# Kernel optimization log

Hardware: AMD Instinct MI355X
Metric: run time of the kernel (lower is better)

The kernel has to match this reference:

```python
import jax, jax.numpy as jnp
import numpy as np

V, D, H, FF, L, ER_LEN = 267, 512, 8, 1024, 6, 2048
HD = D // H
NEG = -1e9


def sinusoidal_pe(S, d, dtype):
    pos = np.arange(S)[:, None].astype(np.float32)
    div = np.exp(np.arange(0, d, 2).astype(np.float32) * (-np.log(10000.0) / d))
    pe = np.zeros((S, d), dtype=np.float32)
    pe[:, 0::2] = np.sin(pos * div)
    pe[:, 1::2] = np.cos(pos * div)
    return jnp.asarray(pe, dtype=dtype)[:, None, :]  # [S,1,D]


def layernorm(x, g, b, eps=1e-5):
    mu = jnp.mean(x, -1, keepdims=True)
    var = jnp.var(x, -1, keepdims=True)
    return (x - mu) * jax.lax.rsqrt(var + eps) * g + b


def skew(qe):
    # qe: [B,H,S,S] -> Music-Transformer skew producing srel [B,H,S,S]
    S = qe.shape[-1]
    mask = jnp.flip(jnp.triu(jnp.ones((S, S), qe.dtype)), axis=0)
    qe = qe * mask
    qe = jnp.pad(qe, ((0, 0), (0, 0), (0, 0), (1, 0)))
    qe = qe.reshape(qe.shape[0], qe.shape[1], S + 1, S)
    return qe[:, :, 1:, :]


def setup_inputs() -> dict:
    key = jax.random.key(0)
    ks = jax.random.split(key, 20)
    s = 0.02
    inp = {
        'inputs_seq': jax.random.randint(ks[0], (2, 2048), 0, V),
        'emb': jax.random.normal(ks[1], (V, D)) * s,
        'in_proj_w': jax.random.normal(ks[2], (L, 3 * D, D)) * s,
        'in_proj_b': jnp.zeros((L, 3 * D)),
        'out_proj_w': jax.random.normal(ks[3], (L, D, D)) * s,
        'out_proj_b': jnp.zeros((L, D)),
        'er': jax.random.normal(ks[4], (L, ER_LEN, HD)) * s,
        'lin1_w': jax.random.normal(ks[5], (L, FF, D)) * s,
        'lin1_b': jnp.zeros((L, FF)),
        'lin2_w': jax.random.normal(ks[6], (L, D, FF)) * s,
        'lin2_b': jnp.zeros((L, D)),
        'ln1_g': jnp.ones((L, D)), 'ln1_b': jnp.zeros((L, D)),
        'ln2_g': jnp.ones((L, D)), 'ln2_b': jnp.zeros((L, D)),
        'fln_g': jnp.ones((D,)), 'fln_b': jnp.zeros((D,)),
        'wout_w': jax.random.normal(ks[7], (V, D)) * s,
        'wout_b': jnp.zeros((V,)),
    }
    return inp


def reference(inputs_seq, emb, in_proj_w, in_proj_b, out_proj_w, out_proj_b, er,
              lin1_w, lin1_b, lin2_w, lin2_b, ln1_g, ln1_b, ln2_g, ln2_b,
              fln_g, fln_b, wout_w, wout_b):
    B, S = inputs_seq.shape
    x = emb[inputs_seq]                       # [B,S,D]
    x = jnp.transpose(x, (1, 0, 2))           # [S,B,D] seq-first
    x = x + sinusoidal_pe(S, D, x.dtype)
    causal = jnp.triu(jnp.full((S, S), NEG, x.dtype), k=1)
    er_start = max(0, ER_LEN - S)
    scale = 1.0 / jnp.sqrt(jnp.asarray(HD, x.dtype))

    for i in range(L):
        qkv = jnp.einsum('sbd,ed->sbe', x, in_proj_w[i]) + in_proj_b[i]
        q, k, v = jnp.split(qkv, 3, axis=-1)
        # [S,B,D] -> [B,H,S,hd]
        def heads(t):
            return jnp.transpose(t.reshape(S, B, H, HD), (1, 2, 0, 3))
        q, k, v = heads(q) * scale, heads(k), heads(v)
        scores = jnp.einsum('bhqd,bhkd->bhqk', q, k)
        qe = jnp.einsum('bhqd,ed->bhqe', q, er[i][er_start:])
        scores = scores + skew(qe) + causal
        attn = jax.nn.softmax(scores, axis=-1)
        ctx = jnp.einsum('bhqk,bhkd->bhqd', attn, v)
        ctx = jnp.transpose(ctx, (2, 0, 1, 3)).reshape(S, B, D)
        attn_out = jnp.einsum('sbd,ed->sbe', ctx, out_proj_w[i]) + out_proj_b[i]
        x = layernorm(x + attn_out, ln1_g[i], ln1_b[i])
        h = jax.nn.relu(jnp.einsum('sbd,fd->sbf', x, lin1_w[i]) + lin1_b[i])
        ff = jnp.einsum('sbf,df->sbd', h, lin2_w[i]) + lin2_b[i]
        x = layernorm(x + ff, ln2_g[i], ln2_b[i])

    x = layernorm(x, fln_g, fln_b)
    return jnp.einsum('sbd,vd->sbv', x, wout_w) + wout_b  # [S,B,V]
```

## Files before the change

### kernel.cpp

```cpp
#include <hip/hip_runtime.h>
#include <hip/hip_bf16.h>

typedef __attribute__((ext_vector_type(4))) float f32x4;
typedef __attribute__((ext_vector_type(8))) short bf16x8;
typedef __attribute__((ext_vector_type(2))) unsigned short u16x2;
typedef __attribute__((ext_vector_type(4))) unsigned short u16x4;
typedef __attribute__((ext_vector_type(8))) unsigned short u16x8;

#define S_LEN 2048
#define BATCH 2
#define DMODEL 512
#define NHEAD 8
#define HDIM 64
#define MROWS 4096
#define LAYERS 6

#define MFMA16(a, b, c) __builtin_amdgcn_mfma_f32_16x16x32_bf16((a), (b), (c), 0, 0, 0)

__device__ __forceinline__ float bf2f(unsigned short u) {
    return __uint_as_float(((unsigned)u) << 16);
}
__device__ __forceinline__ unsigned short f2bf(float f) {
    union { float f; unsigned u; } v; v.f = f;
    unsigned r = v.u + 0x7FFF + ((v.u >> 16) & 1);
    return (unsigned short)(r >> 16);
}
__device__ __forceinline__ bf16x8 load8(const unsigned short* p) {
    return *reinterpret_cast<const bf16x8*>(p);
}

__global__ __launch_bounds__(256) void f2bf_kernel(
    const float* __restrict__ src, unsigned short* __restrict__ dst, int n8)
{
    int i = blockIdx.x * 256 + threadIdx.x;
    if (i >= n8) return;
    f32x4 a = *reinterpret_cast<const f32x4*>(src + (size_t)i * 8);
    f32x4 b = *reinterpret_cast<const f32x4*>(src + (size_t)i * 8 + 4);
    u16x8 o;
#pragma unroll
    for (int j = 0; j < 4; ++j) { o[j] = f2bf(a[j]); o[4 + j] = f2bf(b[j]); }
    *reinterpret_cast<u16x8*>(dst + (size_t)i * 8) = o;
}

__global__ __launch_bounds__(256) void embed_pe_kernel(
    const int* __restrict__ seq, const float* __restrict__ emb,
    float* __restrict__ x, unsigned short* __restrict__ x16)
{
    const int r = blockIdx.x;
    const int j = threadIdx.x;
    const int s = r >> 1, b = r & 1;
    const int tok = seq[b * S_LEN + s];
    const float e0 = emb[(size_t)tok * DMODEL + 2 * j];
    const float e1 = emb[(size_t)tok * DMODEL + 2 * j + 1];
    const double c = -9.210340371976184 / 512.0;
    double dv = exp((double)(2 * j) * c);
    double arg = (double)s * dv;
    const float v0 = e0 + (float)sin(arg);
    const float v1 = e1 + (float)cos(arg);
    x[(size_t)r * DMODEL + 2 * j]     = v0;
    x[(size_t)r * DMODEL + 2 * j + 1] = v1;
    u16x2 o; o[0] = f2bf(v0); o[1] = f2bf(v1);
    *reinterpret_cast<u16x2*>(x16 + (size_t)r * DMODEL + 2 * j) = o;
}

template<int BM>
__global__ __launch_bounds__(256) void gemm_mfma_kernel(
    const unsigned short* __restrict__ A, const unsigned short* __restrict__ W,
    const float* __restrict__ bias,
    float* __restrict__ Cf, unsigned short* __restrict__ Cb,
    unsigned short* __restrict__ vT,
    int N, int K, int relu, int qkvsplit)
{
    constexpr int MF = BM / 32;
    __shared__ __align__(16) unsigned short As[BM * 64];
    __shared__ __align__(16) unsigned short Bs[64 * 64];
    const int tid = threadIdx.x;
    const int w = tid >> 6, lane = tid & 63, l15 = lane & 15, hi = lane >> 4;
    const int wm = w >> 1, wn = w & 1;
    const int n0 = blockIdx.x * 64, m0 = blockIdx.y * BM;
    const int sr = tid >> 3;
    const int ss = tid & 7;

    bf16x8 aprf[MF], bprf[2];
    auto loadA = [&](int k0) {
#pragma unroll
        for (int i = 0; i < MF; ++i) {
            const int r = sr + 32 * i;
            aprf[i] = load8(A + (size_t)(m0 + r) * K + k0 + ((ss ^ ((r >> 1) & 7)) * 8));
        }
    };
    auto loadB = [&](int k0) {
#pragma unroll
        for (int i = 0; i < 2; ++i) {
            const int r = sr + 32 * i;
            const int nn = n0 + r;
            if (nn < N) bprf[i] = load8(W + (size_t)nn * K + k0 + ((ss ^ ((r >> 1) & 7)) * 8));
            else { u16x8 z = {0,0,0,0,0,0,0,0}; bprf[i] = *reinterpret_cast<bf16x8*>(&z); }
        }
    };

    f32x4 acc[MF][2];
#pragma unroll
    for (int mf = 0; mf < MF; ++mf)
#pragma unroll
        for (int nf = 0; nf < 2; ++nf) acc[mf][nf] = f32x4{0.f, 0.f, 0.f, 0.f};

    loadA(0); loadB(0);
    for (int k0 = 0; k0 < K; k0 += 64) {
        __syncthreads();
#pragma unroll
        for (int i = 0; i < MF; ++i)
            *reinterpret_cast<bf16x8*>(As + (sr + 32 * i) * 64 + ss * 8) = aprf[i];
#pragma unroll
        for (int i = 0; i < 2; ++i)
            *reinterpret_cast<bf16x8*>(Bs + (sr + 32 * i) * 64 + ss * 8) = bprf[i];
        if (k0 + 64 < K) { loadA(k0 + 64); loadB(k0 + 64); }
        __syncthreads();

        bf16x8 af[MF][2], bfr[2][2];
#pragma unroll
        for (int mf = 0; mf < MF; ++mf) {
            const int r = wm * (BM / 2) + mf * 16 + l15;
            const int sw = (r >> 1) & 7;
            const unsigned short* base = As + r * 64;
            af[mf][0] = *reinterpret_cast<const bf16x8*>(base + ((hi ^ sw) * 8));
            af[mf][1] = *reinterpret_cast<const bf16x8*>(base + (((hi + 4) ^ sw) * 8));
        }
#pragma unroll
        for (int nf = 0; nf < 2; ++nf) {
            const int r = wn * 32 + nf * 16 + l15;
            const int sw = (r >> 1) & 7;
            const unsigned short* base = Bs + r * 64;
            bfr[nf][0] = *reinterpret_cast<const bf16x8*>(base + ((hi ^ sw) * 8));
            bfr[nf][1] = *reinterpret_cast<const bf16x8*>(base + (((hi + 4) ^ sw) * 8));
        }
#pragma unroll
        for (int mf = 0; mf < MF; ++mf)
#pragma unroll
            for (int nf = 0; nf < 2; ++nf) {
                acc[mf][nf] = MFMA16(af[mf][0], bfr[nf][0], acc[mf][nf]);
                acc[mf][nf] = MFMA16(af[mf][1], bfr[nf][1], acc[mf][nf]);
            }
    }

#pragma unroll
    for (int nf = 0; nf < 2; ++nf) {
        const int col = n0 + wn * 32 + nf * 16 + l15;
        const bool okc = col < N;
        const float bv = okc ? bias[col] : 0.f;
#pragma unroll
        for (int mf = 0; mf < MF; ++mf) {
            const int rbase = m0 + wm * (BM / 2) + mf * 16 + hi * 4;
#pragma unroll
            for (int rg = 0; rg < 4; ++rg) {
                float v = acc[mf][nf][rg] + bv;
                if (relu) v = fmaxf(v, 0.f);
                if (okc) {
                    const int row = rbase + rg;
                    if (qkvsplit) {
                        if (col < 1024) {
                            if (col < 512) v *= 0.125f;
                            Cb[(size_t)row * 1024 + col] = f2bf(v);
                        } else {
                            const int h = (col - 1024) >> 6, d = (col - 1024) & 63;
                            const int s = row >> 1, bb = row & 1;
                            const int kt = s >> 6, kin = s & 63;
                            const int pos = (kin & 3) | (((kin >> 4) & 1) << 2)
                                          | (((kin >> 2) & 3) << 3) | (kin & 32);
                            vT[((((size_t)(bb * 8 + h) * 32 + kt) * 64 + d) << 6) + pos] = f2bf(v);
                        }
                    } else {
                        const size_t idx = (size_t)row * N + col;
                        if (Cb) Cb[idx] = f2bf(v);
                        else    Cf[idx] = v;
                    }
                }
            }
        }
    }
}

__global__ __launch_bounds__(256, 2) void attn_mfma_kernel(
    const unsigned short* __restrict__ qk16, const unsigned short* __restrict__ vT16,
    const unsigned short* __restrict__ er16,
    unsigned short* __restrict__ part16, float* __restrict__ mlbuf)
{
    __shared__ __align__(16) unsigned short K_s[64 * 64];
    __shared__ __align__(16) unsigned short V_T[64 * 64];
    __shared__ __align__(16) unsigned short Er_s[64 * 64];
    __shared__ __align__(16) unsigned short E_w[4 * 16 * 196];

    const int tid  = threadIdx.x;
    const int w    = tid >> 6;
    const int lane = tid & 63;
    const int l15  = lane & 15;
    const int hi   = lane >> 4;
    const int bx   = blockIdx.y;
    const int bh   = blockIdx.x;
    const int b    = bh >> 3, hh = bh & 7;
    const int sk   = lane;
    const int dg0  = w;
    const int dv0  = 16 * w + (lane >> 3);
    const int gv   = lane & 7;

    int qb, c;
    if (bx < 32) { qb = 31 - (bx >> 1); c = bx & 1; }
    else         { qb = 15 - (bx - 32); c = 0; }
    const int pidx = bh * 48 + bx;
    const int q0   = qb * 64;
    const int k0s  = c * 1024;
    const int ntl  = min(qb + 1 - c * 16, 16);
    const int qg   = q0 + 16 * w + l15;

    const unsigned short* qptr = qk16 + ((size_t)qg * BATCH + b) * 1024 + hh * HDIM;
    bf16x8 qf0 = load8(qptr + hi * 8);
    bf16x8 qf1 = load8(qptr + 32 + hi * 8);

    unsigned short* ewp = E_w + (w * 16 + l15) * 196;
    const int E0  = 1984 - q0 + k0s;
    const int E0m = E0 % 192;

#pragma unroll 2
    for (int mf = 0; mf < 8; ++mf) {
        int e = E0 + mf * 16 + l15;
        int ec = e > 2047 ? 2047 : e;
        bf16x8 a0 = load8(er16 + (size_t)ec * 64 + hi * 8);
        bf16x8 a1 = load8(er16 + (size_t)ec * 64 + 32 + hi * 8);
        f32x4 acc = {0.f, 0.f, 0.f, 0.f};
        acc = MFMA16(a0, qf0, acc);
        acc = MFMA16(a1, qf1, acc);
        int col = E0m + mf * 16 + 4 * hi;
        if (col >= 192) col -= 192;
        u16x4 ew;
#pragma unroll
        for (int r = 0; r < 4; ++r) ew[r] = f2bf(acc[r]);
        *reinterpret_cast<u16x4*>(ewp + col) = ew;
    }

    float m = -INFINITY, lsum = 0.f;
    f32x4 acc_o[4];
#pragma unroll
    for (int mf = 0; mf < 4; ++mf) acc_o[mf] = f32x4{0.f, 0.f, 0.f, 0.f};

    int col0t = (2047 - qg + k0s) % 192;

    bf16x8 kpr0, kpr1, vpr0, vpr1, epr0, epr1;
    {
        const unsigned short* krow = qk16 + ((size_t)(k0s + sk) * BATCH + b) * 1024 + 512 + hh * HDIM;
        kpr0 = load8(krow + dg0 * 8);       kpr1 = load8(krow + (dg0 + 4) * 8);
        const unsigned short* vbase = vT16 + (((size_t)bh * 32 + (k0s >> 6)) * 64) * 64;
        vpr0 = load8(vbase + dv0 * 64 + gv * 8);
        vpr1 = load8(vbase + (dv0 + 8) * 64 + gv * 8);
    }
    if (ntl > 1) {
        int e = E0 + 128 + sk;
        int ec = e > 2047 ? 2047 : e;
        epr0 = load8(er16 + (size_t)ec * 64 + dg0 * 8);
        epr1 = load8(er16 + (size_t)ec * 64 + (dg0 + 4) * 8);
    }

    for (int t = 0; t < ntl; ++t) {
        const int k0 = k0s + t * 64;
        const bool doE = (t + 1 < ntl);
        __syncthreads();
        *reinterpret_cast<bf16x8*>(K_s + sk * 64 + ((dg0 ^ (sk & 7)) * 8)) = kpr0;
        *reinterpret_cast<bf16x8*>(K_s + sk * 64 + (((dg0 + 4) ^ (sk & 7)) * 8)) = kpr1;
        *reinterpret_cast<bf16x8*>(V_T + dv0 * 64 + ((gv ^ (dv0 & 7)) * 8)) = vpr0;
        *reinterpret_cast<bf16x8*>(V_T + (dv0 + 8) * 64 + ((gv ^ (dv0 & 7)) * 8)) = vpr1;
        if (doE) {
            *reinterpret_cast<bf16x8*>(Er_s + sk * 64 + ((dg0 ^ (sk & 7)) * 8)) = epr0;
            *reinterpret_cast<bf16x8*>(Er_s + sk * 64 + (((dg0 + 4) ^ (sk & 7)) * 8)) = epr1;
        }
        if (t + 1 < ntl) {
            const unsigned short* krow = qk16 + ((size_t)(k0 + 64 + sk) * BATCH + b) * 1024 + 512 + hh * HDIM;
            kpr0 = load8(krow + dg0 * 8);       kpr1 = load8(krow + (dg0 + 4) * 8);
            const unsigned short* vbase = vT16 + (((size_t)bh * 32 + ((k0 + 64) >> 6)) * 64) * 64;
            vpr0 = load8(vbase + dv0 * 64 + gv * 8);
            vpr1 = load8(vbase + (dv0 + 8) * 64 + gv * 8);
            if (t + 2 < ntl) {
                int e = E0 + 128 + 64 * (t + 1) + sk;
                int ec = e > 2047 ? 2047 : e;
                epr0 = load8(er16 + (size_t)ec * 64 + dg0 * 8);
                epr1 = load8(er16 + (size_t)ec * 64 + (dg0 + 4) * 8);
            }
        }
        __syncthreads();

        f32x4 sacc[4];
#pragma unroll
        for (int f = 0; f < 4; ++f) {
            const int row = l15 + 16 * f;
            bf16x8 ka0 = *reinterpret_cast<const bf16x8*>(K_s + row * 64 + (((0 + hi) ^ (l15 & 7)) * 8));
            bf16x8 ka1 = *reinterpret_cast<const bf16x8*>(K_s + row * 64 + (((4 + hi) ^ (l15 & 7)) * 8));
            f32x4 z = {0.f, 0.f, 0.f, 0.f};
            z = MFMA16(ka0, qf0, z);
            sacc[f] = MFMA16(ka1, qf1, z);
        }

        if (doE) {
            const int fbm = (E0 + 128 + 64 * t) % 192;
#pragma unroll
            for (int mf = 0; mf < 4; ++mf) {
                const int rr = l15 + 16 * mf;
                bf16x8 a0 = *reinterpret_cast<const bf16x8*>(Er_s + rr * 64 + ((hi ^ (l15 & 7)) * 8));
                bf16x8 a1 = *reinterpret_cast<const bf16x8*>(Er_s + rr * 64 + (((hi + 4) ^ (l15 & 7)) * 8));
                f32x4 acc = {0.f, 0.f, 0.f, 0.f};
                acc = MFMA16(a0, qf0, acc);
                acc = MFMA16(a1, qf1, acc);
                int col = fbm + mf * 16 + 4 * hi;
                u16x4 ew;
#pragma unroll
                for (int r = 0; r < 4; ++r) ew[r] = f2bf(acc[r]);
                *reinterpret_cast<u16x4*>(ewp + col) = ew;
            }
        }

        float mt = -INFINITY;
#pragma unroll
        for (int f = 0; f < 4; ++f) {
#pragma unroll
            for (int r = 0; r < 4; ++r) {
                const int kk = 16 * f + 4 * hi + r;
                int col = col0t + kk;
                if (col >= 192) col -= 192;
                float sv = sacc[f][r] + bf2f(ewp[col]);
                if (k0 + kk > qg) sv = -1e9f;
                sacc[f][r] = sv;
                mt = fmaxf(mt, sv);
            }
        }
        mt = fmaxf(mt, __shfl_xor(mt, 16));
        mt = fmaxf(mt, __shfl_xor(mt, 32));
        const float mn = fmaxf(m, mt);
        const float corr = __expf(m - mn);
        float ps = 0.f;
#pragma unroll
        for (int f = 0; f < 4; ++f)
#pragma unroll
            for (int r = 0; r < 4; ++r) {
                const float e = __expf(sacc[f][r] - mn);
                sacc[f][r] = e; ps += e;
            }
        ps += __shfl_xor(ps, 16);
        ps += __shfl_xor(ps, 32);
        lsum = lsum * corr + ps;
        m = mn;

        bf16x8 pf0, pf1;
#pragma unroll
        for (int j = 0; j < 8; ++j) {
            pf0[j] = (short)f2bf(sacc[j >> 2][j & 3]);
            pf1[j] = (short)f2bf(sacc[(j >> 2) + 2][j & 3]);
        }

#pragma unroll
        for (int mf = 0; mf < 4; ++mf) {
            f32x4 a = acc_o[mf];
            a[0] *= corr; a[1] *= corr; a[2] *= corr; a[3] *= corr;
            const unsigned short* vrow = V_T + (l15 + 16 * mf) * 64;
            const int sw = l15 & 7;
            bf16x8 vf0 = *reinterpret_cast<const bf16x8*>(vrow + ((hi ^ sw) * 8));
            bf16x8 vf1 = *reinterpret_cast<const bf16x8*>(vrow + (((4 + hi) ^ sw) * 8));
            a = MFMA16(vf0, pf0, a);
            a = MFMA16(vf1, pf1, a);
            acc_o[mf] = a;
        }

        col0t += 64;
        if (col0t >= 192) col0t -= 192;
    }

    unsigned short* pa = part16 + ((size_t)pidx * 64 + 16 * w + l15) * 64;
#pragma unroll
    for (int mf = 0; mf < 4; ++mf) {
        u16x4 o;
#pragma unroll
        for (int r = 0; r < 4; ++r) o[r] = f2bf(acc_o[mf][r]);
        *reinterpret_cast<u16x4*>(pa + 16 * mf + 4 * hi) = o;
    }
    if (hi == 0) {
        float* ml = mlbuf + ((size_t)pidx * 64 + 16 * w + l15) * 2;
        ml[0] = m; ml[1] = lsum;
    }
}

__global__ __launch_bounds__(256) void attn_combine_kernel(
    const unsigned short* __restrict__ part16, const float* __restrict__ mlbuf,
    unsigned short* __restrict__ ctx16)
{
    const int flat = blockIdx.x * 256 + threadIdx.x;
    const int qi = flat >> 3, dg = flat & 7;
    const int bh = qi >> 11, ql = qi & 2047;
    const int b = bh >> 3, hh = bh & 7;
    const int qb = ql >> 6, rl = ql & 63;

    float o[8];
    u16x8 res;
    if (qb >= 16) {
        const int i0 = bh * 48 + 2 * (31 - qb);
        const int i1 = i0 + 1;
        u16x8 a0 = *reinterpret_cast<const u16x8*>(part16 + ((size_t)i0 * 64 + rl) * 64 + dg * 8);
        u16x8 a1 = *reinterpret_cast<const u16x8*>(part16 + ((size_t)i1 * 64 + rl) * 64 + dg * 8);
        const float* ml0 = mlbuf + ((size_t)i0 * 64 + rl) * 2;
        const float* ml1 = mlbuf + ((size_t)i1 * 64 + rl) * 2;
        const float m0 = ml0[0], l0 = ml0[1], m1 = ml1[0], l1 = ml1[1];
        const float ms = fmaxf(m0, m1);
        const float w0 = __expf(m0 - ms), w1 = __expf(m1 - ms);
        const float inv = 1.f / (l0 * w0 + l1 * w1);
#pragma unroll
        for (int j = 0; j < 8; ++j)
            o[j] = (bf2f(a0[j]) * w0 + bf2f(a1[j]) * w1) * inv;
    } else {
        const int i0 = bh * 48 + 32 + (15 - qb);
        u16x8 a0 = *reinterpret_cast<const u16x8*>(part16 + ((size_t)i0 * 64 + rl) * 64 + dg * 8);
        const float inv = 1.f / mlbuf[((size_t)i0 * 64 + rl) * 2 + 1];
#pragma unroll
        for (int j = 0; j < 8; ++j) o[j] = bf2f(a0[j]) * inv;
    }
#pragma unroll
    for (int j = 0; j < 8; ++j) res[j] = f2bf(o[j]);
    *reinterpret_cast<u16x8*>(ctx16 + ((size_t)ql * BATCH + b) * DMODEL + hh * HDIM + dg * 8) = res;
}

__global__ __launch_bounds__(256) void ln_kernel(
    const float* __restrict__ xin, const float* __restrict__ res,
    const float* __restrict__ gg, const float* __restrict__ bb,
    float* __restrict__ xout, unsigned short* __restrict__ x16out, int has_res)
{
    const int w = threadIdx.x >> 6, lane = threadIdx.x & 63;
    const int row = blockIdx.x * 4 + w;
    const float* xp = xin + (size_t)row * DMODEL + lane * 8;
    f32x4 v0 = *reinterpret_cast<const f32x4*>(xp);
    f32x4 v1 = *reinterpret_cast<const f32x4*>(xp + 4);
    if (has_res) {
        const float* rp = res + (size_t)row * DMODEL + lane * 8;
        v0 += *reinterpret_cast<const f32x4*>(rp);
        v1 += *reinterpret_cast<const f32x4*>(rp + 4);
    }
    float sum = 0.f, ssq = 0.f;
#pragma unroll
    for (int c2 = 0; c2 < 4; ++c2) {
        sum += v0[c2] + v1[c2];
        ssq += v0[c2] * v0[c2] + v1[c2] * v1[c2];
    }
#pragma unroll
    for (int off = 32; off > 0; off >>= 1) {
        sum += __shfl_xor(sum, off);
        ssq += __shfl_xor(ssq, off);
    }
    const float mu = sum * (1.f / 512.f);
    const float var = ssq * (1.f / 512.f) - mu * mu;
    const float rstd = rsqrtf(var + 1e-5f);
    f32x4 g0 = *reinterpret_cast<const f32x4*>(gg + lane * 8);
    f32x4 g1 = *reinterpret_cast<const f32x4*>(gg + lane * 8 + 4);
    f32x4 b0 = *reinterpret_cast<const f32x4*>(bb + lane * 8);
    f32x4 b1 = *reinterpret_cast<const f32x4*>(bb + lane * 8 + 4);
    f32x4 o0, o1;
    u16x8 h;
#pragma unroll
    for (int c2 = 0; c2 < 4; ++c2) {
        o0[c2] = (v0[c2] - mu) * rstd * g0[c2] + b0[c2];
        o1[c2] = (v1[c2] - mu) * rstd * g1[c2] + b1[c2];
        h[c2] = f2bf(o0[c2]); h[4 + c2] = f2bf(o1[c2]);
    }
    float* op = xout + (size_t)row * DMODEL + lane * 8;
    *reinterpret_cast<f32x4*>(op)     = o0;
    *reinterpret_cast<f32x4*>(op + 4) = o1;
    *reinterpret_cast<u16x8*>(x16out + (size_t)row * DMODEL + lane * 8) = h;
}

extern "C" void kernel_launch(void* const* d_in, const int* in_sizes, int n_in,
                              void* d_out, int out_size, void* d_ws, size_t ws_size,
                              hipStream_t stream)
{
    const int*   seq  = (const int*)d_in[0];
    const float* emb  = (const float*)d_in[1];
    const float* ipw  = (const float*)d_in[2];
    const float* ipb  = (const float*)d_in[3];
    const float* opw  = (const float*)d_in[4];
    const float* opb  = (const float*)d_in[5];
    const float* er   = (const float*)d_in[6];
    const float* l1w  = (const float*)d_in[7];
    const float* l1b  = (const float*)d_in[8];
    const float* l2w  = (const float*)d_in[9];
    const float* l2b  = (const float*)d_in[10];
    const float* ln1g = (const float*)d_in[11];
    const float* ln1b = (const float*)d_in[12];
    const float* ln2g = (const float*)d_in[13];
    const float* ln2b = (const float*)d_in[14];
    const float* flng = (const float*)d_in[15];
    const float* flnb = (const float*)d_in[16];
    const float* ww   = (const float*)d_in[17];
    const float* wb   = (const float*)d_in[18];
    float* out = (float*)d_out;

    float* xf  = (float*)d_ws;
    float* tmp = xf + (size_t)MROWS * DMODEL;
    unsigned short* x16   = (unsigned short*)(tmp + (size_t)MROWS * DMODEL);
    unsigned short* qk16  = x16  + (size_t)MROWS * DMODEL;
    unsigned short* ctx16 = qk16 + (size_t)MROWS * 1024;
    unsigned short* er16  = ctx16 + (size_t)MROWS * DMODEL;
    unsigned short* vT16  = er16 + (size_t)LAYERS * S_LEN * HDIM;
    unsigned short* w16   = vT16 + (size_t)16 * 32 * 64 * 64;
    unsigned short* h16   = qk16;
    unsigned short* part16 = (unsigned short*)tmp;
    float* mlbuf = (float*)(part16 + (size_t)768 * 64 * 64);

    unsigned short* ipw16 = w16;
    unsigned short* opw16 = ipw16 + (size_t)LAYERS * 1536 * DMODEL;
    unsigned short* l1w16 = opw16 + (size_t)LAYERS * DMODEL * DMODEL;
    unsigned short* l2w16 = l1w16 + (size_t)LAYERS * 1024 * DMODEL;
    unsigned short* ww16  = l2w16 + (size_t)LAYERS * DMODEL * 1024;

    {
        int n8;
        n8 = LAYERS * 1536 * DMODEL / 8; f2bf_kernel<<<(n8 + 255) / 256, 256, 0, stream>>>(ipw, ipw16, n8);
        n8 = LAYERS * DMODEL * DMODEL / 8; f2bf_kernel<<<(n8 + 255) / 256, 256, 0, stream>>>(opw, opw16, n8);
        n8 = LAYERS * 1024 * DMODEL / 8; f2bf_kernel<<<(n8 + 255) / 256, 256, 0, stream>>>(l1w, l1w16, n8);
        n8 = LAYERS * DMODEL * 1024 / 8; f2bf_kernel<<<(n8 + 255) / 256, 256, 0, stream>>>(l2w, l2w16, n8);
        n8 = 267 * DMODEL / 8;           f2bf_kernel<<<(n8 + 255) / 256, 256, 0, stream>>>(ww, ww16, n8);
        n8 = LAYERS * S_LEN * HDIM / 8;  f2bf_kernel<<<(n8 + 255) / 256, 256, 0, stream>>>(er, er16, n8);
    }

    embed_pe_kernel<<<MROWS, 256, 0, stream>>>(seq, emb, xf, x16);

    for (int i = 0; i < LAYERS; ++i) {
        gemm_mfma_kernel<128><<<dim3(24, 32), 256, 0, stream>>>(
            x16, ipw16 + (size_t)i * 1536 * DMODEL, ipb + (size_t)i * 1536,
            nullptr, qk16, vT16, 1536, DMODEL, 0, 1);
        attn_mfma_kernel<<<dim3(BATCH * NHEAD, 48), 256, 0, stream>>>(
            qk16, vT16, er16 + (size_t)i * S_LEN * HDIM, part16, mlbuf);
        attn_combine_kernel<<<1024, 256, 0, stream>>>(part16, mlbuf, ctx16);
        gemm_mfma_kernel<64><<<dim3(8, 64), 256, 0, stream>>>(
            ctx16, opw16 + (size_t)i * DMODEL * DMODEL, opb + (size_t)i * DMODEL,
            tmp, nullptr, nullptr, DMODEL, DMODEL, 0, 0);
        ln_kernel<<<MROWS / 4, 256, 0, stream>>>(
            xf, tmp, ln1g + (size_t)i * DMODEL, ln1b + (size_t)i * DMODEL, xf, x16, 1);
        gemm_mfma_kernel<128><<<dim3(16, 32), 256, 0, stream>>>(
            x16, l1w16 + (size_t)i * 1024 * DMODEL, l1b + (size_t)i * 1024,
            nullptr, h16, nullptr, 1024, DMODEL, 1, 0);
        gemm_mfma_kernel<64><<<dim3(8, 64), 256, 0, stream>>>(
            h16, l2w16 + (size_t)i * DMODEL * 1024, l2b + (size_t)i * DMODEL,
            tmp, nullptr, nullptr, DMODEL, 1024, 0, 0);
        ln_kernel<<<MROWS / 4, 256, 0, stream>>>(
            xf, tmp, ln2g + (size_t)i * DMODEL, ln2b + (size_t)i * DMODEL, xf, x16, 1);
    }

    ln_kernel<<<MROWS / 4, 256, 0, stream>>>(xf, nullptr, flng, flnb, xf, x16, 0);
    gemm_mfma_kernel<64><<<dim3(5, 64), 256, 0, stream>>>(
        x16, ww16, wb, out, nullptr, nullptr, 267, DMODEL, 0, 0);
}
```

Before: 770.7 us.

## Split attention key range into four 512-key chunks for better load balance

Attention blocks now each cover at most 512 keys (8 tiles) instead of 1024. The grid grows to 80 partial blocks per batch-head, which reduces the imbalance from long causal rows and raises parallelism. The combine kernel becomes a generic online-softmax merge over up to four partials. This costs a larger partial buffer and extra combine traffic, and the partial buffer now extends past the old region into later workspace.

```diff
diff --git a/kernel.cpp b/kernel.cpp
--- a/kernel.cpp
+++ b/kernel.cpp
@@ -204,12 +204,14 @@
     const int gv   = lane & 7;
 
     int qb, c;
-    if (bx < 32) { qb = 31 - (bx >> 1); c = bx & 1; }
-    else         { qb = 15 - (bx - 32); c = 0; }
-    const int pidx = bh * 48 + bx;
+    if (bx < 32)      { qb = 31 - bx;        c = 0; }
+    else if (bx < 56) { qb = 31 - (bx - 32); c = 1; }
+    else if (bx < 72) { qb = 31 - (bx - 56); c = 2; }
+    else              { qb = 31 - (bx - 72); c = 3; }
+    const int pidx = bh * 80 + bx;
     const int q0   = qb * 64;
-    const int k0s  = c * 1024;
-    const int ntl  = min(qb + 1 - c * 16, 16);
+    const int k0s  = c * 512;
+    const int ntl  = min(qb + 1 - c * 8, 8);
     const int qg   = q0 + 16 * w + l15;
 
     const unsigned short* qptr = qk16 + ((size_t)qg * BATCH + b) * 1024 + hh * HDIM;
@@ -394,31 +396,29 @@
     const int b = bh >> 3, hh = bh & 7;
     const int qb = ql >> 6, rl = ql & 63;
 
+    const int nch = (qb >> 3) + 1;
+    float mr = -1e30f, lr = 0.f;
     float o[8];
+#pragma unroll
+    for (int j = 0; j < 8; ++j) o[j] = 0.f;
+
+    for (int cc = 0; cc < nch; ++cc) {
+        const int cb = (cc == 0) ? 0 : (cc == 1) ? 32 : (cc == 2) ? 56 : 72;
+        const int idx = bh * 80 + cb + (31 - qb);
+        const float* ml = mlbuf + ((size_t)idx * 64 + rl) * 2;
+        const float mc = ml[0], lc = ml[1];
+        u16x8 a = *reinterpret_cast<const u16x8*>(part16 + ((size_t)idx * 64 + rl) * 64 + dg * 8);
+        const float mn = fmaxf(mr, mc);
+        const float w0 = __expf(mr - mn), w1 = __expf(mc - mn);
+#pragma unroll
+        for (int j = 0; j < 8; ++j) o[j] = o[j] * w0 + bf2f(a[j]) * w1;
+        lr = lr * w0 + lc * w1;
+        mr = mn;
+    }
+    const float inv = 1.f / lr;
     u16x8 res;
-    if (qb >= 16) {
-        const int i0 = bh * 48 + 2 * (31 - qb);
-        const int i1 = i0 + 1;
-        u16x8 a0 = *reinterpret_cast<const u16x8*>(part16 + ((size_t)i0 * 64 + rl) * 64 + dg * 8);
-        u16x8 a1 = *reinterpret_cast<const u16x8*>(part16 + ((size_t)i1 * 64 + rl) * 64 + dg * 8);
-        const float* ml0 = mlbuf + ((size_t)i0 * 64 + rl) * 2;
-        const float* ml1 = mlbuf + ((size_t)i1 * 64 + rl) * 2;
-        const float m0 = ml0[0], l0 = ml0[1], m1 = ml1[0], l1 = ml1[1];
-        const float ms = fmaxf(m0, m1);
-        const float w0 = __expf(m0 - ms), w1 = __expf(m1 - ms);
-        const float inv = 1.f / (l0 * w0 + l1 * w1);
-#pragma unroll
-        for (int j = 0; j < 8; ++j)
-            o[j] = (bf2f(a0[j]) * w0 + bf2f(a1[j]) * w1) * inv;
-    } else {
-        const int i0 = bh * 48 + 32 + (15 - qb);
-        u16x8 a0 = *reinterpret_cast<const u16x8*>(part16 + ((size_t)i0 * 64 + rl) * 64 + dg * 8);
-        const float inv = 1.f / mlbuf[((size_t)i0 * 64 + rl) * 2 + 1];
-#pragma unroll
-        for (int j = 0; j < 8; ++j) o[j] = bf2f(a0[j]) * inv;
-    }
-#pragma unroll
-    for (int j = 0; j < 8; ++j) res[j] = f2bf(o[j]);
+#pragma unroll
+    for (int j = 0; j < 8; ++j) res[j] = f2bf(o[j] * inv);
     *reinterpret_cast<u16x8*>(ctx16 + ((size_t)ql * BATCH + b) * DMODEL + hh * HDIM + dg * 8) = res;
 }
 
@@ -504,7 +504,7 @@
     unsigned short* w16   = vT16 + (size_t)16 * 32 * 64 * 64;
     unsigned short* h16   = qk16;
     unsigned short* part16 = (unsigned short*)tmp;
-    float* mlbuf = (float*)(part16 + (size_t)768 * 64 * 64);
+    float* mlbuf = (float*)(part16 + (size_t)1280 * 64 * 64);
 
     unsigned short* ipw16 = w16;
     unsigned short* opw16 = ipw16 + (size_t)LAYERS * 1536 * DMODEL;
@@ -528,7 +528,7 @@
         gemm_mfma_kernel<128><<<dim3(24, 32), 256, 0, stream>>>(
             x16, ipw16 + (size_t)i * 1536 * DMODEL, ipb + (size_t)i * 1536,
             nullptr, qk16, vT16, 1536, DMODEL, 0, 1);
-        attn_mfma_kernel<<<dim3(BATCH * NHEAD, 48), 256, 0, stream>>>(
+        attn_mfma_kernel<<<dim3(BATCH * NHEAD, 80), 256, 0, stream>>>(
             qk16, vT16, er16 + (size_t)i * S_LEN * HDIM, part16, mlbuf);
         attn_combine_kernel<<<1024, 256, 0, stream>>>(part16, mlbuf, ctx16);
         gemm_mfma_kernel<64><<<dim3(8, 64), 256, 0, stream>>>(
```

After: 746.9 us. 1.03x faster.
